# Optimization experiments

Hardware: AMD Instinct MI355X
Metric: run time of the kernel (lower is better)

## Reference

```python
import jax, jax.numpy as jnp
import numpy as np

N_HEAD = 16
D_MODEL = 1024
HEAD_DIM = D_MODEL // N_HEAD  # 64
LAMBDA_INIT = 0.8 - 0.6 * float(np.exp(-0.3 * 1))  # layer_depth = 1


def setup_inputs() -> dict:
    key = jax.random.key(0)
    ks = jax.random.split(key, 10)
    B, T, D = 1, 2048, D_MODEL
    std = 0.02
    return {
        "x": jax.random.normal(ks[0], (B, T, D), jnp.float32),
        "Wq": jax.random.normal(ks[1], (D, D), jnp.float32) * std,
        "Wk": jax.random.normal(ks[2], (D, D), jnp.float32) * std,
        "Wv": jax.random.normal(ks[3], (D, D), jnp.float32) * std,
        "Wproj": jax.random.normal(ks[4], (D, D), jnp.float32) * std,
        "lambda_q1": jax.random.normal(ks[5], (HEAD_DIM // 2,), jnp.float32) * 0.1,
        "lambda_k1": jax.random.normal(ks[6], (HEAD_DIM // 2,), jnp.float32) * 0.1,
        "lambda_q2": jax.random.normal(ks[7], (HEAD_DIM // 2,), jnp.float32) * 0.1,
        "lambda_k2": jax.random.normal(ks[8], (HEAD_DIM // 2,), jnp.float32) * 0.1,
    }


def _rms_norm(x):
    # F.rms_norm with no weight: x / sqrt(mean(x^2) + eps)
    eps = jnp.finfo(x.dtype).eps
    return x * jax.lax.rsqrt(jnp.mean(jnp.square(x), axis=-1, keepdims=True) + eps)


def _rotary_cos_sin(T, dim, base=10000.0):
    inv_freq = 1.0 / (base ** (jnp.arange(0, dim, 2, dtype=jnp.float32) / dim))
    freqs = jnp.outer(jnp.arange(T, dtype=jnp.float32), inv_freq)  # [T, dim/2]
    return jnp.cos(freqs), jnp.sin(freqs)


def _apply_rotary(x, cos, sin):
    # x: [B, T, 2, H, hd]; cos/sin: [T, hd/2] broadcast over (group, head)
    d = x.shape[-1] // 2
    c = cos[None, :, None, None, :]
    s = sin[None, :, None, None, :]
    x1, x2 = x[..., :d], x[..., d:]
    return jnp.concatenate([x1 * c + x2 * s, -x1 * s + x2 * c], axis=-1)


def _causal_attn(q, k, v, scale):
    # q,k: [B, T, H, hd]; v: [B, T, H, dv] -> [B, T, H, dv]
    T = q.shape[1]
    scores = jnp.einsum("bthd,bshd->bhts", q, k) * scale  # [B,H,T,T]
    mask = jnp.tril(jnp.ones((T, T), dtype=bool))
    scores = jnp.where(mask, scores, -jnp.inf)
    w = jax.nn.softmax(scores, axis=-1)
    return jnp.einsum("bhts,bshd->bthd", w, v)


def reference(x, Wq, Wk, Wv, Wproj, lambda_q1, lambda_k1, lambda_q2, lambda_k2):
    B, T, D = x.shape
    nh, hd = N_HEAD, HEAD_DIM
    q = (x @ Wq.T).reshape(B, T, 2, nh // 2, hd)
    k = (x @ Wk.T).reshape(B, T, 2, nh // 2, hd)
    v = (x @ Wv.T).reshape(B, T, nh // 2, 2 * hd)

    q, k = _rms_norm(q), _rms_norm(k)
    cos, sin = _rotary_cos_sin(T, hd)
    q, k = _apply_rotary(q, cos, sin), _apply_rotary(k, cos, sin)

    q1, q2 = q[:, :, 0], q[:, :, 1]
    k1, k2 = k[:, :, 0], k[:, :, 1]

    scale = 1.0 / jnp.sqrt(jnp.asarray(hd, x.dtype))
    y1 = _causal_attn(q1, k1, v, scale)  # [B,T,nh/2,2*hd]
    y2 = _causal_attn(q2, k2, v, scale)

    lambda_1 = jnp.exp(jnp.sum(lambda_q1 * lambda_k1))
    lambda_2 = jnp.exp(jnp.sum(lambda_q2 * lambda_k2))
    lambda_full = lambda_1 - lambda_2 + LAMBDA_INIT

    y = (y1 - lambda_full * y2).reshape(B, T, D)
    return y @ Wproj.T
```

## Files before the change

kernel.cpp:

```cpp
#include <hip/hip_runtime.h>
#include <hip/hip_bf16.h>

typedef __attribute__((ext_vector_type(4))) float f32x4;
typedef __attribute__((ext_vector_type(8))) short bf16x8;
typedef unsigned short u16;
typedef unsigned int u32;

#define T_SEQ 2048
#define DMODEL 1024

__device__ __forceinline__ u16 f2bf(float f) {
    __hip_bfloat16 h = __float2bfloat16(f);
    return __builtin_bit_cast(unsigned short, h);
}
__device__ __forceinline__ u16 f2h(float f) {
    _Float16 h = (_Float16)f;
    return __builtin_bit_cast(unsigned short, h);
}
__device__ __forceinline__ float h2f(u16 b) {
    return (float)__builtin_bit_cast(_Float16, b);
}

typedef const void __attribute__((address_space(1))) gvoid_t;
typedef void __attribute__((address_space(3))) lvoid_t;
__device__ __forceinline__ void gload16(const void* g, void* l) {
    __builtin_amdgcn_global_load_lds((gvoid_t*)g, (lvoid_t*)l, 16, 0, 0);
}

__device__ __forceinline__ void cast4(const float* __restrict__ s,
                                      u16* __restrict__ d, int u) {
    int i = u * 4;
    float4 v = *(const float4*)(s + i);
    ushort4 o;
    o.x = f2bf(v.x); o.y = f2bf(v.y); o.z = f2bf(v.z); o.w = f2bf(v.w);
    *(ushort4*)(d + i) = o;
}

__global__ __launch_bounds__(256) void prep(const float* __restrict__ x,
                                            const float* __restrict__ Wq,
                                            const float* __restrict__ Wk,
                                            const float* __restrict__ Wv,
                                            const float* __restrict__ Wp,
                                            u16* __restrict__ x_bf, u16* __restrict__ wq_bf,
                                            u16* __restrict__ wk_bf, u16* __restrict__ wv_bf,
                                            u16* __restrict__ wp_bf,
                                            float* __restrict__ cosT, float* __restrict__ sinT,
                                            const float* __restrict__ lq1, const float* __restrict__ lk1,
                                            const float* __restrict__ lq2, const float* __restrict__ lk2,
                                            float* __restrict__ lam) {
    int b = blockIdx.x;
    if (b < 6144) {
        int u = b * 256 + threadIdx.x;
        if (u < 524288)       cast4(x,  x_bf,  u);
        else if (u < 786432)  cast4(Wq, wq_bf, u - 524288);
        else if (u < 1048576) cast4(Wk, wk_bf, u - 786432);
        else if (u < 1310720) cast4(Wv, wv_bf, u - 1048576);
        else                  cast4(Wp, wp_bf, u - 1310720);
    } else if (b < 6400) {
        int i = (b - 6144) * 256 + threadIdx.x;
        int t = i >> 5, j = i & 31;
        float inv = powf(10000.0f, -(float)j * (1.0f / 32.0f));
        float fr = (float)t * inv;
        cosT[i] = cosf(fr);
        sinT[i] = sinf(fr);
    } else if (threadIdx.x == 0) {
        float s1 = 0.f, s2 = 0.f;
        for (int i = 0; i < 32; ++i) { s1 += lq1[i] * lk1[i]; s2 += lq2[i] * lk2[i]; }
        *lam = expf(s1) - expf(s2) + 0.35550906759096928f;
    }
}

__device__ __forceinline__ void gemm_main64(const u16* __restrict__ A,
                                            const u16* __restrict__ B,
                                            int m0, int n0, int K,
                                            u16* lA, u16* lB, f32x4 acc[2][4]) {
    const int tid = threadIdx.x;
    const int lane = tid & 63;
    const int wid = tid >> 6;
    const int wr = (wid >> 1) * 32;
    const int wc = (wid & 1) * 64;
    const int fr = lane & 15;
    const int kc = lane >> 4;
    const char* Ab = (const char*)A;
    const char* Bb = (const char*)B;
    const int rowbytes = K * 2;
    const int S = K >> 6;

    auto stage = [&](int s, int buf) {
        char* la = (char*)lA + buf * 8192;
        char* lb = (char*)lB + buf * 16384;
#pragma unroll
        for (int i = 0; i < 2; ++i) {
            int seg = i * 256 + tid;
            int row = seg >> 3, cb = (seg & 7) * 16;
            gload16(Ab + (size_t)(m0 + row) * rowbytes + s * 128 + (cb ^ ((row & 7) << 4)),
                    la + seg * 16);
        }
#pragma unroll
        for (int i = 0; i < 4; ++i) {
            int seg = i * 256 + tid;
            int row = seg >> 3, cb = (seg & 7) * 16;
            gload16(Bb + (size_t)(n0 + row) * rowbytes + s * 128 + (cb ^ ((row & 7) << 4)),
                    lb + seg * 16);
        }
    };

    stage(0, 0);
    for (int s = 0; s < S; ++s) {
        const int buf = s & 1;
        if (s + 1 < S) {
            stage(s + 1, buf ^ 1);
            asm volatile("s_waitcnt vmcnt(6)" ::: "memory");
        } else {
            asm volatile("s_waitcnt vmcnt(0)" ::: "memory");
        }
        __builtin_amdgcn_sched_barrier(0);
        __builtin_amdgcn_s_barrier();
        __builtin_amdgcn_sched_barrier(0);

        const char* la = (const char*)lA + buf * 8192;
        const char* lb = (const char*)lB + buf * 16384;
        bf16x8 a[2][2], b[4][2];
#pragma unroll
        for (int m = 0; m < 2; ++m)
#pragma unroll
            for (int kh = 0; kh < 2; ++kh) {
                int row = wr + m * 16 + fr;
                a[m][kh] = *(const bf16x8*)(la + row * 128 +
                                            ((kh * 64 + kc * 16) ^ ((row & 7) << 4)));
            }
#pragma unroll
        for (int n = 0; n < 4; ++n)
#pragma unroll
            for (int kh = 0; kh < 2; ++kh) {
                int row = wc + n * 16 + fr;
                b[n][kh] = *(const bf16x8*)(lb + row * 128 +
                                            ((kh * 64 + kc * 16) ^ ((row & 7) << 4)));
            }
#pragma unroll
        for (int m = 0; m < 2; ++m)
#pragma unroll
            for (int n = 0; n < 4; ++n)
#pragma unroll
                for (int kh = 0; kh < 2; ++kh)
                    acc[m][n] = __builtin_amdgcn_mfma_f32_16x16x32_bf16(a[m][kh], b[n][kh],
                                                                        acc[m][n], 0, 0, 0);
        __builtin_amdgcn_s_barrier();
    }
}

__global__ __launch_bounds__(256) void gemm_qkv(const u16* __restrict__ A,
                                                const u16* __restrict__ wq,
                                                const u16* __restrict__ wk,
                                                const u16* __restrict__ wv,
                                                const float* __restrict__ cosT,
                                                const float* __restrict__ sinT,
                                                u16* __restrict__ q_bf,
                                                u16* __restrict__ k_bf,
                                                u16* __restrict__ vT) {
    __shared__ __align__(16) u16 lA[2 * 64 * 64];
    __shared__ __align__(16) u16 lB[2 * 128 * 64];
    const int nt = blockIdx.x;
    const int which = nt >> 3;
    const u16* B = (which == 0) ? wq : (which == 1) ? wk : wv;
    const int m0 = blockIdx.y * 64;
    const int n0 = (nt & 7) * 128;

    f32x4 acc[2][4] = {};
    gemm_main64(A, B, m0, n0, 1024, lA, lB, acc);

    const int lane = threadIdx.x & 63;
    const int wid = threadIdx.x >> 6;
    const int wr = (wid >> 1) * 32;
    const int wc = (wid & 1) * 64;
    const int fr = lane & 15;
    const int rr = (lane >> 4) * 4;

    if (which == 2) {
#pragma unroll
        for (int m = 0; m < 2; ++m) {
            int t0 = m0 + wr + m * 16 + rr;
#pragma unroll
            for (int n = 0; n < 4; ++n) {
                int cb = n0 + wc + n * 16 + fr;
                ushort4 w;
                w.x = f2bf(acc[m][n][0]);
                w.y = f2bf(acc[m][n][1]);
                w.z = f2bf(acc[m][n][2]);
                w.w = f2bf(acc[m][n][3]);
                *(ushort4*)(vT + (size_t)cb * T_SEQ + t0) = w;
            }
        }
        return;
    }

    const float oscale = (which == 0) ? 0.18033688011112042f : 1.0f;
    const int cb = n0 + wc;
    const int plane = ((cb >> 9) << 3) | ((cb >> 6) & 7);
    u16* dstp = ((which == 0) ? q_bf : k_bf) + (size_t)plane * T_SEQ * 64;
#pragma unroll
    for (int m = 0; m < 2; ++m)
#pragma unroll
        for (int r = 0; r < 4; ++r) {
            int t = m0 + wr + m * 16 + rr + r;
            float s2 = 0.f;
#pragma unroll
            for (int n = 0; n < 4; ++n) { float a = acc[m][n][r]; s2 += a * a; }
            s2 += __shfl_xor(s2, 1); s2 += __shfl_xor(s2, 2);
            s2 += __shfl_xor(s2, 4); s2 += __shfl_xor(s2, 8);
            float inv = rsqrtf(s2 * (1.0f / 64.0f) + 1.1920929e-7f);
#pragma unroll
            for (int n = 0; n < 4; ++n) {
                float a = acc[m][n][r] * inv;
                float p_ = acc[m][n ^ 2][r] * inv;
                int jj = ((n & 1) << 4) + fr;
                float c = cosT[t * 32 + jj], sn = sinT[t * 32 + jj];
                float ov = (n < 2) ? (a * c + p_ * sn) : (a * c - p_ * sn);
                dstp[(size_t)t * 64 + n * 16 + fr] = f2bf(ov * oscale);
            }
        }
}

__global__ __launch_bounds__(256) void gemm_proj(const u16* __restrict__ A,
                                                 const u16* __restrict__ B,
                                                 float* __restrict__ C) {
    __shared__ __align__(16) u16 lA[2 * 64 * 64];
    __shared__ __align__(16) u16 lB[2 * 128 * 64];
    const int m0 = blockIdx.y * 64;
    const int n0 = blockIdx.x * 128;
    f32x4 acc[2][4] = {};
    gemm_main64(A, B, m0, n0, 1024, lA, lB, acc);
    const int lane = threadIdx.x & 63;
    const int wid = threadIdx.x >> 6;
    const int wr = (wid >> 1) * 32;
    const int wc = (wid & 1) * 64;
    const int fr = lane & 15;
    const int rr = (lane >> 4) * 4;
#pragma unroll
    for (int m = 0; m < 2; ++m)
#pragma unroll
        for (int n = 0; n < 4; ++n)
#pragma unroll
            for (int r = 0; r < 4; ++r)
                C[(size_t)(m0 + wr + m * 16 + rr + r) * 1024 + (n0 + wc + n * 16 + fr)] =
                    acc[m][n][r];
}

__global__ __launch_bounds__(256, 6) void attn_kernel(const u16* __restrict__ q_bf,
                                                      const u16* __restrict__ k_bf,
                                                      const u16* __restrict__ vT_bf,
                                                      u16* __restrict__ Oc,
                                                      float2* __restrict__ ml) {
    __shared__ __align__(16) u16 lK[2][32 * 64];
    __shared__ __align__(16) u16 lV[2][64 * 64];

    const int tid = threadIdx.x, lane = tid & 63, wid = tid >> 6;
    const int bid = blockIdx.x;
    const int plane = bid & 15;
    const int u = bid >> 4;
    int qt, chunk;
    if (u < 32)      { qt = 31 - (u >> 2);              chunk = u & 3; }
    else if (u < 56) { int w = u - 32; qt = 23 - w / 3; chunk = w % 3; }
    else if (u < 72) { int w = u - 56; qt = 15 - (w >> 1); chunk = w & 1; }
    else             { qt = 7 - (u - 72);               chunk = 0; }
    const int ntot = 2 * qt + 2;
    const int tb = chunk * 16;
    const int te = min(tb + 16, ntot);
    const int q0 = qt * 64;
    const int h = plane & 7;

    const u16* qp = q_bf + (size_t)plane * T_SEQ * 64;
    const char* kp = (const char*)(k_bf + (size_t)plane * T_SEQ * 64);
    const char* vp = (const char*)(vT_bf + (size_t)h * 128 * T_SEQ);
    const int fr = lane & 15, kc = lane >> 4;
    const int qrow = q0 + wid * 16 + fr;

    bf16x8 aq[2];
#pragma unroll
    for (int kq = 0; kq < 2; ++kq)
        aq[kq] = *(const bf16x8*)(qp + (size_t)qrow * 64 + kq * 32 + kc * 8);

    f32x4 o[8] = {};
    float mi_l = -1e30f, li_l = 0.f;
    const int srcA = fr + ((kc & 1) << 5);
    const int srcB = srcA + 16;
    const bool hi = kc >= 2;

    auto stage = [&](int b, int t) {
        int s0 = t << 5;
        {
            int row = tid >> 3, cp = (tid & 7) * 16;
            gload16(kp + (size_t)(s0 + row) * 128 + (cp ^ ((row & 7) << 4)),
                    (char*)lK[b] + tid * 16);
        }
#pragma unroll
        for (int i = 0; i < 2; ++i) {
            int c = i * 256 + tid;
            int row = c >> 3, cb = (c & 7) * 16;
            int cbs = cb ^ ((row & 7) << 4);
            int d = row * 2 + (cbs >> 6);
            int kk = (cbs & 63) >> 1;
            gload16(vp + (size_t)d * (T_SEQ * 2) + (size_t)(s0 + kk) * 2,
                    (char*)lV[b] + c * 16);
        }
    };

    auto compute = [&](const char* lKb, const char* lVb, int s0, bool diag) {
        f32x4 sacc[2] = {};
        __builtin_amdgcn_s_setprio(1);
#pragma unroll
        for (int kq = 0; kq < 2; ++kq)
#pragma unroll
            for (int n = 0; n < 2; ++n) {
                int row = n * 16 + fr;
                bf16x8 bk = *(const bf16x8*)(lKb + row * 128 +
                                             ((kq * 64 + kc * 16) ^ ((row & 7) << 4)));
                sacc[n] = __builtin_amdgcn_mfma_f32_16x16x32_bf16(bk, aq[kq], sacc[n], 0, 0, 0);
            }
        __builtin_amdgcn_s_setprio(0);

        if (diag) {
#pragma unroll
            for (int n = 0; n < 2; ++n)
#pragma unroll
                for (int r = 0; r < 4; ++r)
                    if (s0 + n * 16 + kc * 4 + r > qrow) sacc[n][r] = -1e30f;
        }
        float rmax = -1e30f;
#pragma unroll
        for (int n = 0; n < 2; ++n)
#pragma unroll
            for (int r = 0; r < 4; ++r)
                rmax = fmaxf(rmax, sacc[n][r]);
        rmax = fmaxf(rmax, __shfl_xor(rmax, 16));
        rmax = fmaxf(rmax, __shfl_xor(rmax, 32));

        bool raise = rmax > mi_l + 8.0f;
        float f = raise ? __builtin_exp2f(mi_l - rmax) : 1.0f;
        if (raise) mi_l = rmax;

        float rs = 0.f;
#pragma unroll
        for (int n = 0; n < 2; ++n)
#pragma unroll
            for (int r = 0; r < 4; ++r) {
                float p = __builtin_exp2f(sacc[n][r] - mi_l);
                sacc[n][r] = p;
                rs += p;
            }
        rs += __shfl_xor(rs, 16);
        rs += __shfl_xor(rs, 32);
        li_l = li_l * f + rs;

        if (__any(raise)) {
#pragma unroll
            for (int n8 = 0; n8 < 8; ++n8)
#pragma unroll
                for (int r = 0; r < 4; ++r) o[n8][r] *= f;
        }

        u32 w32[2][2];
#pragma unroll
        for (int n = 0; n < 2; ++n)
#pragma unroll
            for (int w = 0; w < 2; ++w) {
                u32 rpk;
                asm("v_cvt_pk_bf16_f32 %0, %1, %2"
                    : "=v"(rpk) : "v"(sacc[n][2 * w]), "v"(sacc[n][2 * w + 1]));
                w32[n][w] = rpk;
            }

        u32 a0 = (u32)__shfl((int)w32[0][0], srcA);
        u32 a1 = (u32)__shfl((int)w32[0][1], srcA);
        u32 a2 = (u32)__shfl((int)w32[0][0], srcB);
        u32 a3 = (u32)__shfl((int)w32[0][1], srcB);
        u32 b0 = (u32)__shfl((int)w32[1][0], srcA);
        u32 b1 = (u32)__shfl((int)w32[1][1], srcA);
        u32 b2 = (u32)__shfl((int)w32[1][0], srcB);
        u32 b3 = (u32)__shfl((int)w32[1][1], srcB);
        union { u32 u4[4]; bf16x8 v; } ap;
        ap.u4[0] = hi ? b0 : a0;
        ap.u4[1] = hi ? b1 : a1;
        ap.u4[2] = hi ? b2 : a2;
        ap.u4[3] = hi ? b3 : a3;

        __builtin_amdgcn_s_setprio(1);
#pragma unroll
        for (int n8 = 0; n8 < 8; ++n8) {
            int d = n8 * 16 + fr;
            int row = d >> 1;
            int colb = (d & 1) * 64 + kc * 16;
            bf16x8 bv = *(const bf16x8*)(lVb + row * 128 + (colb ^ ((row & 7) << 4)));
            o[n8] = __builtin_amdgcn_mfma_f32_16x16x32_bf16(bv, ap.v, o[n8], 0, 0, 0);
        }
        __builtin_amdgcn_s_setprio(0);
    };

    stage(0, tb);
    for (int t = tb; t < te; ++t) {
        int ib = (t - tb) & 1;
        if (t + 1 < te) {
            stage(ib ^ 1, t + 1);
            asm volatile("s_waitcnt vmcnt(3)" ::: "memory");
        } else {
            asm volatile("s_waitcnt vmcnt(0)" ::: "memory");
        }
        __builtin_amdgcn_sched_barrier(0);
        __builtin_amdgcn_s_barrier();
        __builtin_amdgcn_sched_barrier(0);
        compute((const char*)lK[ib], (const char*)lV[ib], t << 5, t >= ntot - 2);
        __builtin_amdgcn_s_barrier();
    }

    const float inv_l = 1.0f / li_l;
    u16* Ob = Oc + ((size_t)(plane * 4 + chunk) * T_SEQ + qrow) * 128;
#pragma unroll
    for (int n8 = 0; n8 < 8; ++n8) {
        ushort4 w;
        w.x = f2h(o[n8][0] * inv_l);
        w.y = f2h(o[n8][1] * inv_l);
        w.z = f2h(o[n8][2] * inv_l);
        w.w = f2h(o[n8][3] * inv_l);
        *(ushort4*)(Ob + n8 * 16 + kc * 4) = w;
    }
    if (kc == 0)
        ml[(size_t)(plane * 4 + chunk) * T_SEQ + qrow] = make_float2(mi_l, li_l);
}

__global__ __launch_bounds__(256) void merge_kernel(const u16* __restrict__ Oc,
                                                    const float2* __restrict__ ml,
                                                    const float* __restrict__ lamp,
                                                    u16* __restrict__ yc) {
    int uu = blockIdx.x * 256 + threadIdx.x;
    int t = uu >> 8, rem = uu & 255, h = rem >> 5, d4 = (rem & 31) * 4;
    int qt = t >> 6;
    int nc = (qt + 8) >> 3;
    float lamv = *lamp;
    float yv[2][4];
#pragma unroll
    for (int v = 0; v < 2; ++v) {
        int plane = v * 8 + h;
        float2 m_l[4];
        float M = -1e30f;
#pragma unroll
        for (int c = 0; c < 4; ++c)
            if (c < nc) {
                m_l[c] = ml[(size_t)(plane * 4 + c) * T_SEQ + t];
                M = fmaxf(M, m_l[c].x);
            }
        float den = 0.f, a0 = 0.f, a1 = 0.f, a2 = 0.f, a3 = 0.f;
#pragma unroll
        for (int c = 0; c < 4; ++c)
            if (c < nc) {
                float w = __builtin_exp2f(m_l[c].x - M) * m_l[c].y;
                den += w;
                ushort4 ov = *(const ushort4*)(Oc +
                    ((size_t)(plane * 4 + c) * T_SEQ + t) * 128 + d4);
                a0 += w * h2f(ov.x);
                a1 += w * h2f(ov.y);
                a2 += w * h2f(ov.z);
                a3 += w * h2f(ov.w);
            }
        float inv = 1.0f / den;
        yv[v][0] = a0 * inv; yv[v][1] = a1 * inv;
        yv[v][2] = a2 * inv; yv[v][3] = a3 * inv;
    }
    ushort4 o;
    o.x = f2bf(yv[0][0] - lamv * yv[1][0]);
    o.y = f2bf(yv[0][1] - lamv * yv[1][1]);
    o.z = f2bf(yv[0][2] - lamv * yv[1][2]);
    o.w = f2bf(yv[0][3] - lamv * yv[1][3]);
    *(ushort4*)(yc + (size_t)t * 1024 + h * 128 + d4) = o;
}

extern "C" void kernel_launch(void* const* d_in, const int* in_sizes, int n_in,
                              void* d_out, int out_size, void* d_ws, size_t ws_size,
                              hipStream_t stream) {
    const float* x   = (const float*)d_in[0];
    const float* Wq  = (const float*)d_in[1];
    const float* Wk  = (const float*)d_in[2];
    const float* Wv  = (const float*)d_in[3];
    const float* Wp  = (const float*)d_in[4];
    const float* lq1 = (const float*)d_in[5];
    const float* lk1 = (const float*)d_in[6];
    const float* lq2 = (const float*)d_in[7];
    const float* lk2 = (const float*)d_in[8];
    float* out = (float*)d_out;

    char* ws = (char*)d_ws;
    u16*    x_bf  = (u16*)(ws);
    u16*    wq_bf = (u16*)(ws + (4ull << 20));
    u16*    wk_bf = (u16*)(ws + (6ull << 20));
    u16*    wv_bf = (u16*)(ws + (8ull << 20));
    u16*    wp_bf = (u16*)(ws + (10ull << 20));
    u16*    vT_bf = (u16*)(ws + (12ull << 20));
    u16*    q_bf  = (u16*)(ws + (16ull << 20));
    u16*    k_bf  = (u16*)(ws + (20ull << 20));
    u16*    Oc    = (u16*)(ws + (24ull << 20));
    float2* ml    = (float2*)(ws + (56ull << 20));
    u16*    yc_bf = (u16*)(ws + (57ull << 20));
    float*  cosT  = (float*)(ws + (61ull << 20));
    float*  sinT  = (float*)(ws + (61ull << 20) + (256ull << 10));
    float*  lam   = (float*)(ws + (61ull << 20) + (512ull << 10));

    prep<<<6401, 256, 0, stream>>>(x, Wq, Wk, Wv, Wp,
                                   x_bf, wq_bf, wk_bf, wv_bf, wp_bf,
                                   cosT, sinT, lq1, lk1, lq2, lk2, lam);

    gemm_qkv<<<dim3(24, 32), 256, 0, stream>>>(x_bf, wq_bf, wk_bf, wv_bf,
                                               cosT, sinT, q_bf, k_bf, vT_bf);

    attn_kernel<<<1280, 256, 0, stream>>>(q_bf, k_bf, vT_bf, Oc, ml);

    merge_kernel<<<2048, 256, 0, stream>>>(Oc, ml, lam, yc_bf);

    gemm_proj<<<dim3(8, 32), 256, 0, stream>>>(yc_bf, wp_bf, out);
}
```

Baseline: 90.70 us.

## Double attention query tile to 128 rows per block to reuse K/V tiles

Each wave now handles two 16-row query groups, so one block covers 128 query rows instead of 64. Every K/V tile staged in LDS feeds twice as many MFMAs, which halves global K/V traffic and the per-block staging and barrier overhead. The grid shrinks from 1280 to 640 blocks and the chunk split and merge count are rederived for 128-row tiles. The cost is roughly double the accumulator registers, a launch-bounds occupancy hint lowered from 6 to 4, fewer blocks to spread over the CUs, and more wasted work on the causal diagonal.

```diff
diff --git a/kernel.cpp b/kernel.cpp
--- a/kernel.cpp
+++ b/kernel.cpp
@@ -246,7 +246,7 @@
                     acc[m][n][r];
 }
 
-__global__ __launch_bounds__(256, 6) void attn_kernel(const u16* __restrict__ q_bf,
+__global__ __launch_bounds__(256, 4) void attn_kernel(const u16* __restrict__ q_bf,
                                                       const u16* __restrict__ k_bf,
                                                       const u16* __restrict__ vT_bf,
                                                       u16* __restrict__ Oc,
@@ -259,29 +259,31 @@
     const int plane = bid & 15;
     const int u = bid >> 4;
     int qt, chunk;
-    if (u < 32)      { qt = 31 - (u >> 2);              chunk = u & 3; }
-    else if (u < 56) { int w = u - 32; qt = 23 - w / 3; chunk = w % 3; }
-    else if (u < 72) { int w = u - 56; qt = 15 - (w >> 1); chunk = w & 1; }
-    else             { qt = 7 - (u - 72);               chunk = 0; }
-    const int ntot = 2 * qt + 2;
+    if (u < 16)      { qt = 15 - (u >> 2);              chunk = u & 3; }
+    else if (u < 28) { int w = u - 16; qt = 11 - w / 3; chunk = w % 3; }
+    else if (u < 36) { int w = u - 28; qt = 7 - (w >> 1); chunk = w & 1; }
+    else             { qt = 3 - (u - 36);               chunk = 0; }
+    const int ntot = 4 * qt + 4;
     const int tb = chunk * 16;
     const int te = min(tb + 16, ntot);
-    const int q0 = qt * 64;
+    const int q0 = qt * 128;
     const int h = plane & 7;
 
     const u16* qp = q_bf + (size_t)plane * T_SEQ * 64;
     const char* kp = (const char*)(k_bf + (size_t)plane * T_SEQ * 64);
     const char* vp = (const char*)(vT_bf + (size_t)h * 128 * T_SEQ);
     const int fr = lane & 15, kc = lane >> 4;
-    const int qrow = q0 + wid * 16 + fr;
-
-    bf16x8 aq[2];
-#pragma unroll
-    for (int kq = 0; kq < 2; ++kq)
-        aq[kq] = *(const bf16x8*)(qp + (size_t)qrow * 64 + kq * 32 + kc * 8);
-
-    f32x4 o[8] = {};
-    float mi_l = -1e30f, li_l = 0.f;
+    const int qrow0 = q0 + wid * 32 + fr;
+
+    bf16x8 aq[2][2];
+#pragma unroll
+    for (int g = 0; g < 2; ++g)
+#pragma unroll
+        for (int kq = 0; kq < 2; ++kq)
+            aq[g][kq] = *(const bf16x8*)(qp + (size_t)(qrow0 + g * 16) * 64 + kq * 32 + kc * 8);
+
+    f32x4 o[2][8] = {};
+    float mi[2] = {-1e30f, -1e30f}, li[2] = {0.f, 0.f};
     const int srcA = fr + ((kc & 1) << 5);
     const int srcB = srcA + 16;
     const bool hi = kc >= 2;
@@ -306,83 +308,97 @@
     };
 
     auto compute = [&](const char* lKb, const char* lVb, int s0, bool diag) {
-        f32x4 sacc[2] = {};
-        __builtin_amdgcn_s_setprio(1);
+        bf16x8 bk[2][2];
 #pragma unroll
         for (int kq = 0; kq < 2; ++kq)
 #pragma unroll
             for (int n = 0; n < 2; ++n) {
                 int row = n * 16 + fr;
-                bf16x8 bk = *(const bf16x8*)(lKb + row * 128 +
+                bk[kq][n] = *(const bf16x8*)(lKb + row * 128 +
                                              ((kq * 64 + kc * 16) ^ ((row & 7) << 4)));
-                sacc[n] = __builtin_amdgcn_mfma_f32_16x16x32_bf16(bk, aq[kq], sacc[n], 0, 0, 0);
-            }
+            }
+        f32x4 sacc[2][2] = {};
+        __builtin_amdgcn_s_setprio(1);
+#pragma unroll
+        for (int g = 0; g < 2; ++g)
+#pragma unroll
+            for (int kq = 0; kq < 2; ++kq)
+#pragma unroll
+                for (int n = 0; n < 2; ++n)
+                    sacc[g][n] = __builtin_amdgcn_mfma_f32_16x16x32_bf16(bk[kq][n], aq[g][kq],
+                                                                         sacc[g][n], 0, 0, 0);
         __builtin_amdgcn_s_setprio(0);
 
-        if (diag) {
+        u32 w32[2][2][2];
+#pragma unroll
+        for (int g = 0; g < 2; ++g) {
+            const int qrow = qrow0 + g * 16;
+            if (diag) {
+#pragma unroll
+                for (int n = 0; n < 2; ++n)
+#pragma unroll
+                    for (int r = 0; r < 4; ++r)
+                        if (s0 + n * 16 + kc * 4 + r > qrow) sacc[g][n][r] = -1e30f;
+            }
+            float rmax = -1e30f;
 #pragma unroll
             for (int n = 0; n < 2; ++n)
 #pragma unroll
                 for (int r = 0; r < 4; ++r)
-                    if (s0 + n * 16 + kc * 4 + r > qrow) sacc[n][r] = -1e30f;
-        }
-        float rmax = -1e30f;
-#pragma unroll
-        for (int n = 0; n < 2; ++n)
-#pragma unroll
-            for (int r = 0; r < 4; ++r)
-                rmax = fmaxf(rmax, sacc[n][r]);
-        rmax = fmaxf(rmax, __shfl_xor(rmax, 16));
-        rmax = fmaxf(rmax, __shfl_xor(rmax, 32));
-
-        bool raise = rmax > mi_l + 8.0f;
-        float f = raise ? __builtin_exp2f(mi_l - rmax) : 1.0f;
-        if (raise) mi_l = rmax;
-
-        float rs = 0.f;
-#pragma unroll
-        for (int n = 0; n < 2; ++n)
-#pragma unroll
-            for (int r = 0; r < 4; ++r) {
-                float p = __builtin_exp2f(sacc[n][r] - mi_l);
-                sacc[n][r] = p;
-                rs += p;
-            }
-        rs += __shfl_xor(rs, 16);
-        rs += __shfl_xor(rs, 32);
-        li_l = li_l * f + rs;
-
-        if (__any(raise)) {
-#pragma unroll
-            for (int n8 = 0; n8 < 8; ++n8)
-#pragma unroll
-                for (int r = 0; r < 4; ++r) o[n8][r] *= f;
-        }
-
-        u32 w32[2][2];
-#pragma unroll
-        for (int n = 0; n < 2; ++n)
-#pragma unroll
-            for (int w = 0; w < 2; ++w) {
-                u32 rpk;
-                asm("v_cvt_pk_bf16_f32 %0, %1, %2"
-                    : "=v"(rpk) : "v"(sacc[n][2 * w]), "v"(sacc[n][2 * w + 1]));
-                w32[n][w] = rpk;
-            }
-
-        u32 a0 = (u32)__shfl((int)w32[0][0], srcA);
-        u32 a1 = (u32)__shfl((int)w32[0][1], srcA);
-        u32 a2 = (u32)__shfl((int)w32[0][0], srcB);
-        u32 a3 = (u32)__shfl((int)w32[0][1], srcB);
-        u32 b0 = (u32)__shfl((int)w32[1][0], srcA);
-        u32 b1 = (u32)__shfl((int)w32[1][1], srcA);
-        u32 b2 = (u32)__shfl((int)w32[1][0], srcB);
-        u32 b3 = (u32)__shfl((int)w32[1][1], srcB);
-        union { u32 u4[4]; bf16x8 v; } ap;
-        ap.u4[0] = hi ? b0 : a0;
-        ap.u4[1] = hi ? b1 : a1;
-        ap.u4[2] = hi ? b2 : a2;
-        ap.u4[3] = hi ? b3 : a3;
+                    rmax = fmaxf(rmax, sacc[g][n][r]);
+            rmax = fmaxf(rmax, __shfl_xor(rmax, 16));
+            rmax = fmaxf(rmax, __shfl_xor(rmax, 32));
+
+            bool raise = rmax > mi[g] + 8.0f;
+            float f = raise ? __builtin_exp2f(mi[g] - rmax) : 1.0f;
+            if (raise) mi[g] = rmax;
+
+            float rs = 0.f;
+#pragma unroll
+            for (int n = 0; n < 2; ++n)
+#pragma unroll
+                for (int r = 0; r < 4; ++r) {
+                    float p = __builtin_exp2f(sacc[g][n][r] - mi[g]);
+                    sacc[g][n][r] = p;
+                    rs += p;
+                }
+            rs += __shfl_xor(rs, 16);
+            rs += __shfl_xor(rs, 32);
+            li[g] = li[g] * f + rs;
+
+            if (__any(raise)) {
+#pragma unroll
+                for (int n8 = 0; n8 < 8; ++n8)
+#pragma unroll
+                    for (int r = 0; r < 4; ++r) o[g][n8][r] *= f;
+            }
+#pragma unroll
+            for (int n = 0; n < 2; ++n)
+#pragma unroll
+                for (int w = 0; w < 2; ++w) {
+                    u32 rpk;
+                    asm("v_cvt_pk_bf16_f32 %0, %1, %2"
+                        : "=v"(rpk) : "v"(sacc[g][n][2 * w]), "v"(sacc[g][n][2 * w + 1]));
+                    w32[g][n][w] = rpk;
+                }
+        }
+
+        union { u32 u4[4]; bf16x8 v; } ap[2];
+#pragma unroll
+        for (int g = 0; g < 2; ++g) {
+            u32 a0 = (u32)__shfl((int)w32[g][0][0], srcA);
+            u32 a1 = (u32)__shfl((int)w32[g][0][1], srcA);
+            u32 a2 = (u32)__shfl((int)w32[g][0][0], srcB);
+            u32 a3 = (u32)__shfl((int)w32[g][0][1], srcB);
+            u32 b0 = (u32)__shfl((int)w32[g][1][0], srcA);
+            u32 b1 = (u32)__shfl((int)w32[g][1][1], srcA);
+            u32 b2 = (u32)__shfl((int)w32[g][1][0], srcB);
+            u32 b3 = (u32)__shfl((int)w32[g][1][1], srcB);
+            ap[g].u4[0] = hi ? b0 : a0;
+            ap[g].u4[1] = hi ? b1 : a1;
+            ap[g].u4[2] = hi ? b2 : a2;
+            ap[g].u4[3] = hi ? b3 : a3;
+        }
 
         __builtin_amdgcn_s_setprio(1);
 #pragma unroll
@@ -391,7 +407,8 @@
             int row = d >> 1;
             int colb = (d & 1) * 64 + kc * 16;
             bf16x8 bv = *(const bf16x8*)(lVb + row * 128 + (colb ^ ((row & 7) << 4)));
-            o[n8] = __builtin_amdgcn_mfma_f32_16x16x32_bf16(bv, ap.v, o[n8], 0, 0, 0);
+            o[0][n8] = __builtin_amdgcn_mfma_f32_16x16x32_bf16(bv, ap[0].v, o[0][n8], 0, 0, 0);
+            o[1][n8] = __builtin_amdgcn_mfma_f32_16x16x32_bf16(bv, ap[1].v, o[1][n8], 0, 0, 0);
         }
         __builtin_amdgcn_s_setprio(0);
     };
@@ -408,23 +425,26 @@
         __builtin_amdgcn_sched_barrier(0);
         __builtin_amdgcn_s_barrier();
         __builtin_amdgcn_sched_barrier(0);
-        compute((const char*)lK[ib], (const char*)lV[ib], t << 5, t >= ntot - 2);
+        compute((const char*)lK[ib], (const char*)lV[ib], t << 5, t >= ntot - 4);
         __builtin_amdgcn_s_barrier();
     }
 
-    const float inv_l = 1.0f / li_l;
-    u16* Ob = Oc + ((size_t)(plane * 4 + chunk) * T_SEQ + qrow) * 128;
-#pragma unroll
-    for (int n8 = 0; n8 < 8; ++n8) {
-        ushort4 w;
-        w.x = f2h(o[n8][0] * inv_l);
-        w.y = f2h(o[n8][1] * inv_l);
-        w.z = f2h(o[n8][2] * inv_l);
-        w.w = f2h(o[n8][3] * inv_l);
-        *(ushort4*)(Ob + n8 * 16 + kc * 4) = w;
+#pragma unroll
+    for (int g = 0; g < 2; ++g) {
+        const float inv_l = 1.0f / li[g];
+        u16* Ob = Oc + ((size_t)(plane * 4 + chunk) * T_SEQ + qrow0 + g * 16) * 128;
+#pragma unroll
+        for (int n8 = 0; n8 < 8; ++n8) {
+            ushort4 w;
+            w.x = f2h(o[g][n8][0] * inv_l);
+            w.y = f2h(o[g][n8][1] * inv_l);
+            w.z = f2h(o[g][n8][2] * inv_l);
+            w.w = f2h(o[g][n8][3] * inv_l);
+            *(ushort4*)(Ob + n8 * 16 + kc * 4) = w;
+        }
+        if (kc == 0)
+            ml[(size_t)(plane * 4 + chunk) * T_SEQ + qrow0 + g * 16] = make_float2(mi[g], li[g]);
     }
-    if (kc == 0)
-        ml[(size_t)(plane * 4 + chunk) * T_SEQ + qrow] = make_float2(mi_l, li_l);
 }
 
 __global__ __launch_bounds__(256) void merge_kernel(const u16* __restrict__ Oc,
@@ -433,8 +453,8 @@
                                                     u16* __restrict__ yc) {
     int uu = blockIdx.x * 256 + threadIdx.x;
     int t = uu >> 8, rem = uu & 255, h = rem >> 5, d4 = (rem & 31) * 4;
-    int qt = t >> 6;
-    int nc = (qt + 8) >> 3;
+    int qt = t >> 7;
+    int nc = (4 * qt + 19) >> 4;
     float lamv = *lamp;
     float yv[2][4];
 #pragma unroll
@@ -510,7 +530,7 @@
     gemm_qkv<<<dim3(24, 32), 256, 0, stream>>>(x_bf, wq_bf, wk_bf, wv_bf,
                                                cosT, sinT, q_bf, k_bf, vT_bf);
 
-    attn_kernel<<<1280, 256, 0, stream>>>(q_bf, k_bf, vT_bf, Oc, ml);
+    attn_kernel<<<640, 256, 0, stream>>>(q_bf, k_bf, vT_bf, Oc, ml);
 
     merge_kernel<<<2048, 256, 0, stream>>>(Oc, ml, lam, yc_bf);
 
```

Result: slower. 105.9 us (+16.8%).
